# Optimization experiments

Hardware: AMD Instinct MI355X
Metric: run time of the kernel (lower is better)

Reference implementation:

```python
import jax, jax.numpy as jnp
import numpy as np

INPUT_DIM = 256
EMBED_DIM = 256
NUM_HEADS = 8
HEAD_DIM = EMBED_DIM // NUM_HEADS
N_TOKENS = 11136
N_BATCH = 16


def _xavier(key, shape):
    fan_out, fan_in = shape
    bound = np.sqrt(6.0 / (fan_in + fan_out)).astype(np.float32)
    return jax.random.uniform(key, shape, jnp.float32, -bound, bound)


def setup_inputs() -> dict:
    key = jax.random.key(0)
    k_x, k_ids, k_qkv, k_o = jax.random.split(key, 4)
    x = jax.random.normal(k_x, (N_TOKENS, INPUT_DIM), jnp.float32)
    batch_ids = jnp.sort(jax.random.randint(k_ids, (N_TOKENS,), 0, N_BATCH)).astype(jnp.int32)
    qkv_w = _xavier(k_qkv, (3 * EMBED_DIM, INPUT_DIM))
    qkv_b = jnp.zeros((3 * EMBED_DIM,), jnp.float32)
    o_w = _xavier(k_o, (EMBED_DIM, EMBED_DIM))
    o_b = jnp.zeros((EMBED_DIM,), jnp.float32)
    return {"x": x, "batch_ids": batch_ids, "qkv_w": qkv_w, "qkv_b": qkv_b,
            "o_w": o_w, "o_b": o_b}


def reference(x, batch_ids, qkv_w, qkv_b, o_w, o_b):
    # batch_ids is concrete metadata (mirrors np.unique on CPU in the original).
    ids = np.asarray(batch_ids)
    vals, counts = np.unique(ids, return_counts=True)
    B = len(vals)
    S = int(counts.max())
    offsets = np.concatenate([np.zeros(1, np.int64), np.cumsum(counts)[:-1]])
    seg = np.searchsorted(vals, ids)               # segment index per token
    pos = np.arange(ids.shape[0]) - offsets[seg]   # position within segment

    qkv = x @ qkv_w.T + qkv_b                      # [N, 3E]
    # pad_sequence with padding_value=1 -> scatter tokens into an all-ones buffer
    fin = jnp.ones((B, S, 3 * EMBED_DIM), qkv.dtype).at[seg, pos].set(qkv)
    # padded rows sum to exactly 3E (all ones) -> mask True marks padding
    pad_mask = fin.sum(-1) >= fin.shape[-1]        # [B, S]

    qkv4 = fin.reshape(B, S, NUM_HEADS, 3 * HEAD_DIM).transpose(0, 2, 1, 3)
    q, k, v = jnp.split(qkv4, 3, axis=-1)          # each [B, H, S, hd]

    logits = jnp.einsum('bhqd,bhkd->bhqk', q, k) * (HEAD_DIM ** -0.5)
    logits = jnp.where(pad_mask[:, None, None, :], -jnp.inf, logits)
    attn = jax.nn.softmax(logits, axis=-1)         # [B, H, S, S]

    out = jnp.einsum('bhqk,bhkd->bhqd', attn, v)
    out = out.transpose(0, 2, 1, 3).reshape(B, S, EMBED_DIM)
    out = out[seg, pos]                            # unpad -> [N, E]
    return out @ o_w.T + o_b
```

## Files before the change

### kernel.cpp

```cpp
#include <hip/hip_runtime.h>
#include <stdint.h>


#define N_TOK 11136
#define E 256
#define H 8
#define HD 32

typedef __attribute__((ext_vector_type(8))) __bf16 bf16x8;
typedef __attribute__((ext_vector_type(8))) unsigned short u16x8;
typedef __attribute__((ext_vector_type(4))) float f32x4;

__device__ __forceinline__ unsigned short f2bf(float f) {
  unsigned int u = __float_as_uint(f);
  u = (u + 0x7FFFu + ((u >> 16) & 1u)) >> 16;
  return (unsigned short)u;
}
__device__ __forceinline__ float bf2f(unsigned short s) {
  return __uint_as_float(((unsigned int)s) << 16);
}
__device__ __forceinline__ bf16x8 ld8(const unsigned short* p) {
  return *(const bf16x8*)p;
}

__global__ void k_split(const float* __restrict__ x, const float* __restrict__ qw,
                        const float* __restrict__ ow, const int* __restrict__ ids,
                        unsigned short* __restrict__ xhi, unsigned short* __restrict__ xlo,
                        unsigned short* __restrict__ whi, unsigned short* __restrict__ wlo,
                        unsigned short* __restrict__ owb, int* __restrict__ offs) {
  if (blockIdx.x == 0 && threadIdx.x < 17) {
    int b = threadIdx.x, lo = 0, hi = N_TOK;
    while (lo < hi) { int mid = (lo + hi) >> 1; if (ids[mid] < b) lo = mid + 1; else hi = mid; }
    offs[b] = lo;
  }
  const int NX4 = N_TOK * E / 4;
  const int NW4 = 3 * E * E / 4;
  const int NO4 = E * E / 4;
  int total = NX4 + NW4 + NO4;
  for (int i = blockIdx.x * blockDim.x + threadIdx.x; i < total;
       i += gridDim.x * blockDim.x) {
    if (i < NX4) {
      float4 v = ((const float4*)x)[i];
      ushort4 hv, lv;
      hv.x = f2bf(v.x); lv.x = f2bf(v.x - bf2f(hv.x));
      hv.y = f2bf(v.y); lv.y = f2bf(v.y - bf2f(hv.y));
      hv.z = f2bf(v.z); lv.z = f2bf(v.z - bf2f(hv.z));
      hv.w = f2bf(v.w); lv.w = f2bf(v.w - bf2f(hv.w));
      ((ushort4*)xhi)[i] = hv; ((ushort4*)xlo)[i] = lv;
    } else if (i < NX4 + NW4) {
      int j = i - NX4;
      float4 v = ((const float4*)qw)[j];
      ushort4 hv, lv;
      hv.x = f2bf(v.x); lv.x = f2bf(v.x - bf2f(hv.x));
      hv.y = f2bf(v.y); lv.y = f2bf(v.y - bf2f(hv.y));
      hv.z = f2bf(v.z); lv.z = f2bf(v.z - bf2f(hv.z));
      hv.w = f2bf(v.w); lv.w = f2bf(v.w - bf2f(hv.w));
      ((ushort4*)whi)[j] = hv; ((ushort4*)wlo)[j] = lv;
    } else {
      int j = i - NX4 - NW4;
      float4 v = ((const float4*)ow)[j];
      ushort4 hv;
      hv.x = f2bf(v.x); hv.y = f2bf(v.y); hv.z = f2bf(v.z); hv.w = f2bf(v.w);
      ((ushort4*)owb)[j] = hv;
    }
  }
}

#define QK_BSTRIDE 264
#define QSCALE (0.17677669529663687f * 1.4426950408889634f)
__global__ __launch_bounds__(256, 3) void k_qkv(
    const unsigned short* __restrict__ xhi, const unsigned short* __restrict__ xlo,
    const unsigned short* __restrict__ whi, const unsigned short* __restrict__ wlo,
    const float* __restrict__ qkv_b,
    unsigned short* __restrict__ Qb, unsigned short* __restrict__ Kb,
    unsigned short* __restrict__ Vt) {
  int bid = blockIdx.x + 16 * blockIdx.y;
  int xcd = bid & 7;
  int j8 = bid >> 3;
  int colb = j8 & 15;
  int tile = (j8 >> 4) * 8 + xcd;
  if (tile >= 58) return;
  int col0 = colb * 48;
  __shared__ __align__(16) unsigned short Bhi[48 * QK_BSTRIDE];
  __shared__ __align__(16) unsigned short Blo[48 * QK_BSTRIDE];
  int tid = threadIdx.x;
  int w = tid >> 6, lane = tid & 63, m = lane & 15, quad = lane >> 4;
  int rowb = tile * 192 + w * 48;

  {
    const u16x8* wh8 = (const u16x8*)(whi + (size_t)col0 * E);
    const u16x8* wl8 = (const u16x8*)(wlo + (size_t)col0 * E);
#pragma unroll
    for (int i = 0; i < 6; ++i) {
      int flat = i * 256 + tid;
      int row = flat >> 5, c8 = flat & 31;
      *(u16x8*)(Bhi + row * QK_BSTRIDE + c8 * 8) = wh8[flat];
      *(u16x8*)(Blo + row * QK_BSTRIDE + c8 * 8) = wl8[flat];
    }
  }
  __syncthreads();

  f32x4 acc[3][3] = {};
  bf16x8 ahn[3], aln[3];
#pragma unroll
  for (int mt = 0; mt < 3; ++mt) {
    const size_t ro = (size_t)(rowb + mt * 16 + m) * E + quad * 8;
    ahn[mt] = ld8(xhi + ro);
    aln[mt] = ld8(xlo + ro);
  }
  for (int kc = 0; kc < 8; ++kc) {
    bf16x8 ah[3], al[3];
#pragma unroll
    for (int mt = 0; mt < 3; ++mt) { ah[mt] = ahn[mt]; al[mt] = aln[mt]; }
    int kon = (kc < 7 ? kc + 1 : kc) * 32 + quad * 8;
#pragma unroll
    for (int mt = 0; mt < 3; ++mt) {
      const size_t ro = (size_t)(rowb + mt * 16 + m) * E + kon;
      ahn[mt] = ld8(xhi + ro);
      aln[mt] = ld8(xlo + ro);
    }
    int ko = kc * 32 + quad * 8;
#pragma unroll
    for (int t = 0; t < 3; ++t) {
      bf16x8 bh = ld8(Bhi + (16 * t + m) * QK_BSTRIDE + ko);
      bf16x8 bl = ld8(Blo + (16 * t + m) * QK_BSTRIDE + ko);
#pragma unroll
      for (int mt = 0; mt < 3; ++mt) {
        acc[mt][t] = __builtin_amdgcn_mfma_f32_16x16x32_bf16(ah[mt], bh, acc[mt][t], 0, 0, 0);
        acc[mt][t] = __builtin_amdgcn_mfma_f32_16x16x32_bf16(ah[mt], bl, acc[mt][t], 0, 0, 0);
        acc[mt][t] = __builtin_amdgcn_mfma_f32_16x16x32_bf16(al[mt], bh, acc[mt][t], 0, 0, 0);
      }
    }
  }
#pragma unroll
  for (int t = 0; t < 3; ++t) {
    int j = col0 + 16 * t + m;
    int hd = j / 96;
    int rr = j - hd * 96;
    float bias = qkv_b[j];
#pragma unroll
    for (int mt = 0; mt < 3; ++mt) {
      int tokb = rowb + mt * 16 + quad * 4;
      if (rr < 64) {
        float qsc = (rr < 32) ? QSCALE : 1.0f;
        unsigned short* dst = (rr < 32) ? (Qb + (size_t)hd * N_TOK * HD + rr)
                                        : (Kb + (size_t)hd * N_TOK * HD + (rr - 32));
#pragma unroll
        for (int r = 0; r < 4; ++r)
          dst[(size_t)(tokb + r) * HD] = f2bf((acc[mt][t][r] + bias) * qsc);
      } else {
        int d = rr - 64;
        ushort4 pk;
        pk.x = f2bf(acc[mt][t][0] + bias); pk.y = f2bf(acc[mt][t][1] + bias);
        pk.z = f2bf(acc[mt][t][2] + bias); pk.w = f2bf(acc[mt][t][3] + bias);
        *(ushort4*)(Vt + (size_t)(hd * HD + d) * N_TOK + tokb) = pk;
      }
    }
  }
}

#define PSTRIDE 72
#define VSTR 72
__global__ __launch_bounds__(256, 4) void k_attn(
    const int* __restrict__ ids, const int* __restrict__ offs,
    const unsigned short* __restrict__ Qb, const unsigned short* __restrict__ Kb,
    const unsigned short* __restrict__ Vt,
    unsigned short* __restrict__ attnb) {
  __shared__ __align__(16) unsigned short Kl[2][64 * 32];
  __shared__ __align__(16) unsigned short Vl[2][32 * VSTR];
  __shared__ __align__(16) unsigned short ldsP[4][16 * PSTRIDE];
  __shared__ int bred[8];
  int tid = threadIdx.x;
  int w = tid >> 6, lane = tid & 63;
  int m = lane & 15, quad = lane >> 4;
  int h = blockIdx.x;
  int tok0 = blockIdx.y * 64;
  int q0 = tok0 + w * 16;
  unsigned short* P = ldsP[w];
  int tok = q0 + m;
  int b = ids[tok];
  int st = offs[b], en = offs[b + 1];
  int kmin = st, kmax = en, stM = st, enm = en;
#pragma unroll
  for (int d = 1; d <= 8; d <<= 1) {
    kmin = min(kmin, __shfl_xor(kmin, d));
    kmax = max(kmax, __shfl_xor(kmax, d));
    stM  = max(stM,  __shfl_xor(stM,  d));
    enm  = min(enm,  __shfl_xor(enm,  d));
  }
  if (lane == 0) { bred[w] = kmin; bred[4 + w] = kmax; }
  __syncthreads();
  int kminB = min(min(bred[0], bred[1]), min(bred[2], bred[3]));
  int kmaxB = max(max(bred[4], bred[5]), max(bred[6], bred[7]));
  int k0beg = kminB & ~63;

  const unsigned short* Kbase = Kb + (size_t)h * N_TOK * HD;
  const unsigned short* Vbase = Vt + (size_t)h * HD * N_TOK;
  bf16x8 qf = ld8(Qb + (size_t)(h * N_TOK + tok) * HD + quad * 8);

  int krow = w * 16 + (lane >> 2);
  int kgof = (lane & 3) * 8;
  int vrow = w * 8 + (lane >> 3);
  int vgof = (lane & 7) * 8;

  bf16x8 kg = ld8(Kbase + (size_t)(k0beg + krow) * HD + kgof);
  bf16x8 vg = ld8(Vbase + (size_t)vrow * N_TOK + k0beg + vgof);
  *(bf16x8*)(&Kl[0][krow * 32 + kgof]) = kg;
  *(bf16x8*)(&Vl[0][vrow * VSTR + vgof]) = vg;
  __syncthreads();

  float lsum = 0.f;
  f32x4 o0 = {}, o1 = {};
  int buf = 0;
  for (int k0 = k0beg; k0 < kmaxB; k0 += 64) {
    int k1 = (k0 + 64 < kmaxB) ? (k0 + 64) : k0;
    kg = ld8(Kbase + (size_t)(k1 + krow) * HD + kgof);
    vg = ld8(Vbase + (size_t)vrow * N_TOK + k1 + vgof);
    const unsigned short* Kc = &Kl[buf][0];
    const unsigned short* Vc = &Vl[buf][0];
    f32x4 s[4];
#pragma unroll
    for (int i = 0; i < 4; ++i) {
      bf16x8 kf = ld8(Kc + (16 * i + m) * 32 + quad * 8);
      f32x4 z = {};
      s[i] = __builtin_amdgcn_mfma_f32_16x16x32_bf16(kf, qf, z, 0, 0, 0);
    }
    bool interior = (k0 >= stM && k0 + 64 <= enm);
    int jb = k0 + quad * 4;
#pragma unroll
    for (int i = 0; i < 4; ++i) {
      float p[4];
#pragma unroll
      for (int r = 0; r < 4; ++r) {
        float sv = s[i][r];
        if (!interior) {
          int j = jb + 16 * i + r;
          sv = (j >= st && j < en) ? sv : -3e38f;
        }
        float e;
        asm("v_exp_f32 %0, %1" : "=v"(e) : "v"(sv));
        p[r] = e;
      }
      lsum += (p[0] + p[1]) + (p[2] + p[3]);
      unsigned int b0 = __float_as_uint(p[0]) + 0x8000u;
      unsigned int b1 = __float_as_uint(p[1]) + 0x8000u;
      unsigned int b2 = __float_as_uint(p[2]) + 0x8000u;
      unsigned int b3 = __float_as_uint(p[3]) + 0x8000u;
      uint2 pk;
      pk.x = (b1 & 0xFFFF0000u) | (b0 >> 16);
      pk.y = (b3 & 0xFFFF0000u) | (b2 >> 16);
      *(uint2*)(P + m * PSTRIDE + 16 * i + quad * 4) = pk;
    }
#pragma unroll
    for (int c = 0; c < 2; ++c) {
      bf16x8 pf  = ld8(P + m * PSTRIDE + 32 * c + quad * 8);
      bf16x8 vf0 = ld8(Vc + m * VSTR + 32 * c + quad * 8);
      bf16x8 vf1 = ld8(Vc + (16 + m) * VSTR + 32 * c + quad * 8);
      o0 = __builtin_amdgcn_mfma_f32_16x16x32_bf16(vf0, pf, o0, 0, 0, 0);
      o1 = __builtin_amdgcn_mfma_f32_16x16x32_bf16(vf1, pf, o1, 0, 0, 0);
    }
    *(bf16x8*)(&Kl[buf ^ 1][krow * 32 + kgof]) = kg;
    *(bf16x8*)(&Vl[buf ^ 1][vrow * VSTR + vgof]) = vg;
    __syncthreads();
    buf ^= 1;
  }
  lsum += __shfl_xor(lsum, 16);
  lsum += __shfl_xor(lsum, 32);
  float inv = 1.0f / lsum;
  ushort4 pk0, pk1;
  pk0.x = f2bf(o0[0] * inv); pk0.y = f2bf(o0[1] * inv);
  pk0.z = f2bf(o0[2] * inv); pk0.w = f2bf(o0[3] * inv);
  pk1.x = f2bf(o1[0] * inv); pk1.y = f2bf(o1[1] * inv);
  pk1.z = f2bf(o1[2] * inv); pk1.w = f2bf(o1[3] * inv);
  *(ushort4*)(attnb + (size_t)tok * E + h * HD + quad * 4) = pk0;
  *(ushort4*)(attnb + (size_t)tok * E + h * HD + 16 + quad * 4) = pk1;
}

__global__ __launch_bounds__(256, 4) void k_oproj(
    const unsigned short* __restrict__ attnb, const unsigned short* __restrict__ owb,
    const float* __restrict__ ob, float* __restrict__ out) {
  __shared__ __align__(16) unsigned short Bo[64 * QK_BSTRIDE];
  int tid = threadIdx.x;
  int w = tid >> 6, lane = tid & 63, m = lane & 15, quad = lane >> 4;
  int tok0 = blockIdx.x * 64, col0 = blockIdx.y * 64;
  {
    const u16x8* o8 = (const u16x8*)(owb + (size_t)col0 * E);
#pragma unroll
    for (int i = 0; i < 8; ++i) {
      int flat = i * 256 + tid;
      int row = flat >> 5, c8 = flat & 31;
      *(u16x8*)(Bo + row * QK_BSTRIDE + c8 * 8) = o8[flat];
    }
  }
  __syncthreads();
  f32x4 acc[4] = {};
  int arow = tok0 + 16 * w + m;
  const unsigned short* abase = attnb + (size_t)arow * E + quad * 8;
  bf16x8 an = ld8(abase);
  for (int kc = 0; kc < 8; ++kc) {
    bf16x8 a = an;
    an = ld8(abase + (kc < 7 ? kc + 1 : kc) * 32);
    int ko = kc * 32 + quad * 8;
#pragma unroll
    for (int t = 0; t < 4; ++t) {
      bf16x8 b = ld8(Bo + (16 * t + m) * QK_BSTRIDE + ko);
      acc[t] = __builtin_amdgcn_mfma_f32_16x16x32_bf16(a, b, acc[t], 0, 0, 0);
    }
  }
#pragma unroll
  for (int t = 0; t < 4; ++t) {
    int j = col0 + 16 * t + m;
    float bias = ob[j];
#pragma unroll
    for (int r = 0; r < 4; ++r) {
      int tok = tok0 + 16 * w + quad * 4 + r;
      out[(size_t)tok * E + j] = acc[t][r] + bias;
    }
  }
}

extern "C" void kernel_launch(void* const* d_in, const int* in_sizes, int n_in,
                              void* d_out, int out_size, void* d_ws, size_t ws_size,
                              hipStream_t stream) {
  const float* x   = (const float*)d_in[0];
  const int*   ids = (const int*)d_in[1];
  const float* qw  = (const float*)d_in[2];
  const float* qb  = (const float*)d_in[3];
  const float* ow  = (const float*)d_in[4];
  const float* ob  = (const float*)d_in[5];
  float* out = (float*)d_out;

  char* p = (char*)d_ws;
  auto alloc = [&](size_t bytes) {
    char* r = p;
    p += (bytes + 255) & ~(size_t)255;
    return r;
  };
  int* offs = (int*)alloc(32 * sizeof(int));
  unsigned short* xhi = (unsigned short*)alloc((size_t)N_TOK * E * 2);
  unsigned short* xlo = (unsigned short*)alloc((size_t)N_TOK * E * 2);
  unsigned short* whi = (unsigned short*)alloc((size_t)3 * E * E * 2);
  unsigned short* wlo = (unsigned short*)alloc((size_t)3 * E * E * 2);
  unsigned short* owb = (unsigned short*)alloc((size_t)E * E * 2);
  unsigned short* Qb  = (unsigned short*)alloc((size_t)N_TOK * E * 2);
  unsigned short* Kb  = (unsigned short*)alloc((size_t)N_TOK * E * 2);
  unsigned short* Vt  = (unsigned short*)alloc((size_t)N_TOK * E * 2);
  unsigned short* att = (unsigned short*)alloc((size_t)N_TOK * E * 2);

  k_split<<<dim3(1712), dim3(256), 0, stream>>>(x, qw, ow, ids, xhi, xlo, whi, wlo, owb, offs);
  k_qkv<<<dim3(16, 64), dim3(256), 0, stream>>>(xhi, xlo, whi, wlo, qb, Qb, Kb, Vt);
  k_attn<<<dim3(H, N_TOK / 64), dim3(256), 0, stream>>>(ids, offs, Qb, Kb, Vt, att);
  k_oproj<<<dim3(N_TOK / 64, E / 64), dim3(256), 0, stream>>>(att, owb, ob, out);
}
```

Before: 154.7 us.

## Deepen global prefetch, use packed bf16 convert, add MFMA priority hints

The QKV projection and output projection GEMMs now prefetch A fragments two k-chunks ahead instead of one, so global load latency is hidden for longer. The attention kernel replaces the manual rounding and bit-packing of probabilities and outputs with the hardware v_cvt_pk_bf16_f32 instruction. It also wraps the MFMA sections in s_setprio raises so matrix work is issued ahead of other waves. The deeper prefetch costs extra VGPRs, which may lower occupancy, and the hardware convert may round differently from the old add-0x8000 truncation.

```diff
diff --git a/kernel.cpp b/kernel.cpp
--- a/kernel.cpp
+++ b/kernel.cpp
@@ -21,6 +21,11 @@
 }
 __device__ __forceinline__ bf16x8 ld8(const unsigned short* p) {
   return *(const bf16x8*)p;
+}
+__device__ __forceinline__ unsigned int cvtpk(float a, float b) {
+  unsigned int r;
+  asm("v_cvt_pk_bf16_f32 %0, %1, %2" : "=v"(r) : "v"(a), "v"(b));
+  return r;
 }
 
 __global__ void k_split(const float* __restrict__ x, const float* __restrict__ qw,
@@ -101,23 +106,27 @@
   __syncthreads();
 
   f32x4 acc[3][3] = {};
-  bf16x8 ahn[3], aln[3];
+  bf16x8 ah1[3], al1[3], ah2[3], al2[3];
 #pragma unroll
   for (int mt = 0; mt < 3; ++mt) {
     const size_t ro = (size_t)(rowb + mt * 16 + m) * E + quad * 8;
-    ahn[mt] = ld8(xhi + ro);
-    aln[mt] = ld8(xlo + ro);
+    ah1[mt] = ld8(xhi + ro);       al1[mt] = ld8(xlo + ro);
+    ah2[mt] = ld8(xhi + ro + 32);  al2[mt] = ld8(xlo + ro + 32);
   }
   for (int kc = 0; kc < 8; ++kc) {
     bf16x8 ah[3], al[3];
 #pragma unroll
-    for (int mt = 0; mt < 3; ++mt) { ah[mt] = ahn[mt]; al[mt] = aln[mt]; }
-    int kon = (kc < 7 ? kc + 1 : kc) * 32 + quad * 8;
+    for (int mt = 0; mt < 3; ++mt) {
+      ah[mt] = ah1[mt]; al[mt] = al1[mt];
+      ah1[mt] = ah2[mt]; al1[mt] = al2[mt];
+    }
+    int kn = kc + 2; if (kn > 7) kn = 7;
+    int kon = kn * 32 + quad * 8;
 #pragma unroll
     for (int mt = 0; mt < 3; ++mt) {
       const size_t ro = (size_t)(rowb + mt * 16 + m) * E + kon;
-      ahn[mt] = ld8(xhi + ro);
-      aln[mt] = ld8(xlo + ro);
+      ah2[mt] = ld8(xhi + ro);
+      al2[mt] = ld8(xlo + ro);
     }
     int ko = kc * 32 + quad * 8;
 #pragma unroll
@@ -219,12 +228,14 @@
     const unsigned short* Kc = &Kl[buf][0];
     const unsigned short* Vc = &Vl[buf][0];
     f32x4 s[4];
+    __builtin_amdgcn_s_setprio(1);
 #pragma unroll
     for (int i = 0; i < 4; ++i) {
       bf16x8 kf = ld8(Kc + (16 * i + m) * 32 + quad * 8);
       f32x4 z = {};
       s[i] = __builtin_amdgcn_mfma_f32_16x16x32_bf16(kf, qf, z, 0, 0, 0);
     }
+    __builtin_amdgcn_s_setprio(0);
     bool interior = (k0 >= stM && k0 + 64 <= enm);
     int jb = k0 + quad * 4;
 #pragma unroll
@@ -242,15 +253,12 @@
         p[r] = e;
       }
       lsum += (p[0] + p[1]) + (p[2] + p[3]);
-      unsigned int b0 = __float_as_uint(p[0]) + 0x8000u;
-      unsigned int b1 = __float_as_uint(p[1]) + 0x8000u;
-      unsigned int b2 = __float_as_uint(p[2]) + 0x8000u;
-      unsigned int b3 = __float_as_uint(p[3]) + 0x8000u;
       uint2 pk;
-      pk.x = (b1 & 0xFFFF0000u) | (b0 >> 16);
-      pk.y = (b3 & 0xFFFF0000u) | (b2 >> 16);
+      pk.x = cvtpk(p[0], p[1]);
+      pk.y = cvtpk(p[2], p[3]);
       *(uint2*)(P + m * PSTRIDE + 16 * i + quad * 4) = pk;
     }
+    __builtin_amdgcn_s_setprio(1);
 #pragma unroll
     for (int c = 0; c < 2; ++c) {
       bf16x8 pf  = ld8(P + m * PSTRIDE + 32 * c + quad * 8);
@@ -259,6 +267,7 @@
       o0 = __builtin_amdgcn_mfma_f32_16x16x32_bf16(vf0, pf, o0, 0, 0, 0);
       o1 = __builtin_amdgcn_mfma_f32_16x16x32_bf16(vf1, pf, o1, 0, 0, 0);
     }
+    __builtin_amdgcn_s_setprio(0);
     *(bf16x8*)(&Kl[buf ^ 1][krow * 32 + kgof]) = kg;
     *(bf16x8*)(&Vl[buf ^ 1][vrow * VSTR + vgof]) = vg;
     __syncthreads();
@@ -267,13 +276,13 @@
   lsum += __shfl_xor(lsum, 16);
   lsum += __shfl_xor(lsum, 32);
   float inv = 1.0f / lsum;
-  ushort4 pk0, pk1;
-  pk0.x = f2bf(o0[0] * inv); pk0.y = f2bf(o0[1] * inv);
-  pk0.z = f2bf(o0[2] * inv); pk0.w = f2bf(o0[3] * inv);
-  pk1.x = f2bf(o1[0] * inv); pk1.y = f2bf(o1[1] * inv);
-  pk1.z = f2bf(o1[2] * inv); pk1.w = f2bf(o1[3] * inv);
-  *(ushort4*)(attnb + (size_t)tok * E + h * HD + quad * 4) = pk0;
-  *(ushort4*)(attnb + (size_t)tok * E + h * HD + 16 + quad * 4) = pk1;
+  uint2 s0, s1;
+  s0.x = cvtpk(o0[0] * inv, o0[1] * inv);
+  s0.y = cvtpk(o0[2] * inv, o0[3] * inv);
+  s1.x = cvtpk(o1[0] * inv, o1[1] * inv);
+  s1.y = cvtpk(o1[2] * inv, o1[3] * inv);
+  *(uint2*)(attnb + (size_t)tok * E + h * HD + quad * 4) = s0;
+  *(uint2*)(attnb + (size_t)tok * E + h * HD + 16 + quad * 4) = s1;
 }
 
 __global__ __launch_bounds__(256, 4) void k_oproj(
@@ -296,10 +305,13 @@
   f32x4 acc[4] = {};
   int arow = tok0 + 16 * w + m;
   const unsigned short* abase = attnb + (size_t)arow * E + quad * 8;
-  bf16x8 an = ld8(abase);
+  bf16x8 a1 = ld8(abase);
+  bf16x8 a2 = ld8(abase + 32);
   for (int kc = 0; kc < 8; ++kc) {
-    bf16x8 a = an;
-    an = ld8(abase + (kc < 7 ? kc + 1 : kc) * 32);
+    bf16x8 a = a1;
+    a1 = a2;
+    int kn = kc + 2; if (kn > 7) kn = 7;
+    a2 = ld8(abase + kn * 32);
     int ko = kc * 32 + quad * 8;
 #pragma unroll
     for (int t = 0; t < 4; ++t) {
```

Result: no change. 151.9 us (-1.8%).
